# Optimization experiments

Measured on AMD Instinct MI355X. Metric: run time of the kernel, lower is better.

The kernel has to match this reference:

```python
import jax, jax.numpy as jnp
import numpy as np

NUM_HEADS = 8
HIDDEN_DIM = 64
N_REAL = 30000
N_VIRT = 2000
N_NODES = N_REAL + N_VIRT
N_EDGES = 512000
VOCAB = 100000


def setup_inputs() -> dict:
    key = jax.random.key(0)
    k1, k2, k3, k4, k5 = jax.random.split(key, 5)
    features = jax.random.normal(k1, (VOCAB, HIDDEN_DIM), dtype=jnp.float32)
    virtue_emb = jax.random.normal(k2, (N_VIRT, HIDDEN_DIM), dtype=jnp.float32)  # nn.Embedding weight ~ N(0,1)
    cnodes = jax.random.randint(k3, (N_REAL,), 0, VOCAB, dtype=jnp.int64)
    src = jax.random.randint(k4, (N_EDGES,), 0, N_NODES, dtype=jnp.int64)
    dst = jax.random.randint(k5, (N_EDGES,), 0, N_NODES, dtype=jnp.int64)
    vm_idx = jnp.arange(N_VIRT, dtype=jnp.int64) + N_REAL  # virtual nodes are appended after real nodes
    return {"features": features, "virtue_emb": virtue_emb, "cnodes": cnodes,
            "src": src, "dst": dst, "vm_idx": vm_idx}


def _edge_softmax(e, dst, n_nodes):
    # DGL edge_softmax: softmax over incoming edges of each destination node.
    m = jax.ops.segment_max(e, dst, num_segments=n_nodes)          # [N,H,1]
    ex = jnp.exp(e - m[dst])                                       # [E,H,1]
    s = jax.ops.segment_sum(ex, dst, num_segments=n_nodes)        # [N,H,1]
    return ex / s[dst]


def reference(features, virtue_emb, cnodes, src, dst, vm_idx):
    real_ndata = features[cnodes]                                  # [R,D] F.embedding
    ndata = jnp.concatenate([real_ndata, virtue_emb], axis=0)      # [N,D]
    n = ndata.shape[0]
    # agg_type='neighbor': cat([h]*H, dim=1).view(-1,H,D) == broadcast along head dim
    nft = jnp.broadcast_to(ndata[:, None, :], (n, NUM_HEADS, HIDDEN_DIM))
    e = jnp.ones((src.shape[0], NUM_HEADS, 1), dtype=ndata.dtype)
    eft = _edge_softmax(e, dst, n)                                 # [E,H,1]
    new_nft = jax.ops.segment_sum(nft[src] * eft, dst, num_segments=n)      # round 1: u_mul_e / sum
    final_nft = jax.ops.segment_sum(new_nft[src] * eft, dst, num_segments=n)  # round 2
    return final_nft[vm_idx]                                       # [V,H,D]
```

## Files before the change

### kernel.cpp

```cpp
#include <hip/hip_runtime.h>

constexpr int HEADS  = 8;
constexpr int DIM    = 64;
constexpr int NREAL  = 30000;
constexpr int NVIRT  = 2000;
constexpr int NNODES = NREAL + NVIRT;
constexpr int NEDGES = 512000;
constexpr int STRIDE = 64;


__global__ __launch_bounds__(256) void k_prep(const float* __restrict__ features,
                                              const float* __restrict__ virtue,
                                              const int* __restrict__ cnodes,
                                              const int* __restrict__ src,
                                              const int* __restrict__ dst,
                                              float* __restrict__ ndata,
                                              int* __restrict__ cnt,
                                              unsigned short* __restrict__ slots) {
  int i = blockIdx.x * blockDim.x + threadIdx.x;
  {
    int node = i >> 4;
    int q    = i & 15;
    const float4* srcp = (node < NREAL)
        ? (const float4*)(features + (long)cnodes[node] * DIM)
        : (const float4*)(virtue + (long)(node - NREAL) * DIM);
    ((float4*)(ndata + (long)node * DIM))[q] = srcp[q];
  }
  {
    int d = dst[i];
    int pos = atomicAdd(&cnt[d], 1);
    if (pos < STRIDE) slots[(long)d * STRIDE + pos] = (unsigned short)src[i];
  }
}

__global__ __launch_bounds__(256) void k_agg1(const int* __restrict__ cnt,
                                              const unsigned short* __restrict__ slots,
                                              const float* __restrict__ ndata,
                                              float* __restrict__ new_nft) {
  int node = blockIdx.x * 4 + (threadIdx.x >> 6);
  if (node >= NNODES) return;
  int lane = threadIdx.x & 63;
  int q = lane >> 4;
  int l = lane & 15;
  int deg = cnt[node];
  if (deg > STRIDE) deg = STRIDE;
  int myidx = 0;
  if (lane < deg) myidx = (int)slots[(long)node * STRIDE + lane];
  float4 acc  = make_float4(0.f, 0.f, 0.f, 0.f);
  float4 acc2 = make_float4(0.f, 0.f, 0.f, 0.f);
  const float4* nd4 = (const float4*)ndata;
  for (int k0 = 0; k0 < deg; k0 += 8) {
    int ka = k0 + q;
    int kb = k0 + q + 4;
    int sa = __shfl(myidx, ka);
    int sb = __shfl(myidx, kb);
    if (ka < deg) {
      float4 v = nd4[(long)sa * 16 + l];
      acc.x += v.x; acc.y += v.y; acc.z += v.z; acc.w += v.w;
    }
    if (kb < deg) {
      float4 v = nd4[(long)sb * 16 + l];
      acc2.x += v.x; acc2.y += v.y; acc2.z += v.z; acc2.w += v.w;
    }
  }
  acc.x += acc2.x; acc.y += acc2.y; acc.z += acc2.z; acc.w += acc2.w;
  acc.x += __shfl_xor(acc.x, 16); acc.y += __shfl_xor(acc.y, 16);
  acc.z += __shfl_xor(acc.z, 16); acc.w += __shfl_xor(acc.w, 16);
  acc.x += __shfl_xor(acc.x, 32); acc.y += __shfl_xor(acc.y, 32);
  acc.z += __shfl_xor(acc.z, 32); acc.w += __shfl_xor(acc.w, 32);
  if (q == 0) {
    float inv = (deg > 0) ? 1.0f / (float)deg : 0.0f;
    acc.x *= inv; acc.y *= inv; acc.z *= inv; acc.w *= inv;
    ((float4*)new_nft)[(long)node * 16 + l] = acc;
  }
}

__global__ __launch_bounds__(256) void k_agg2(const int* __restrict__ cnt,
                                              const unsigned short* __restrict__ slots,
                                              const float* __restrict__ new_nft,
                                              float* __restrict__ out) {
  int v = blockIdx.x * 4 + (threadIdx.x >> 6);
  if (v >= NVIRT) return;
  int node = NREAL + v;
  int lane = threadIdx.x & 63;
  int q = lane >> 4;
  int l = lane & 15;
  int deg = cnt[node];
  if (deg > STRIDE) deg = STRIDE;
  int myidx = 0;
  if (lane < deg) myidx = (int)slots[(long)node * STRIDE + lane];
  float4 acc  = make_float4(0.f, 0.f, 0.f, 0.f);
  float4 acc2 = make_float4(0.f, 0.f, 0.f, 0.f);
  const float4* nf4 = (const float4*)new_nft;
  for (int k0 = 0; k0 < deg; k0 += 8) {
    int ka = k0 + q;
    int kb = k0 + q + 4;
    int sa = __shfl(myidx, ka);
    int sb = __shfl(myidx, kb);
    if (ka < deg) {
      float4 x = nf4[(long)sa * 16 + l];
      acc.x += x.x; acc.y += x.y; acc.z += x.z; acc.w += x.w;
    }
    if (kb < deg) {
      float4 x = nf4[(long)sb * 16 + l];
      acc2.x += x.x; acc2.y += x.y; acc2.z += x.z; acc2.w += x.w;
    }
  }
  acc.x += acc2.x; acc.y += acc2.y; acc.z += acc2.z; acc.w += acc2.w;
  acc.x += __shfl_xor(acc.x, 16); acc.y += __shfl_xor(acc.y, 16);
  acc.z += __shfl_xor(acc.z, 16); acc.w += __shfl_xor(acc.w, 16);
  acc.x += __shfl_xor(acc.x, 32); acc.y += __shfl_xor(acc.y, 32);
  acc.z += __shfl_xor(acc.z, 32); acc.w += __shfl_xor(acc.w, 32);
  if (q == 0) {
    float inv = (deg > 0) ? 1.0f / (float)deg : 0.0f;
    acc.x *= inv; acc.y *= inv; acc.z *= inv; acc.w *= inv;
    float4* o4 = (float4*)out;
#pragma unroll
    for (int h = 0; h < HEADS; ++h)
      o4[((long)v * HEADS + h) * 16 + l] = acc;
  }
}


extern "C" void kernel_launch(void* const* d_in, const int* in_sizes, int n_in,
                              void* d_out, int out_size, void* d_ws, size_t ws_size,
                              hipStream_t stream) {
  const float* features = (const float*)d_in[0];
  const float* virtue   = (const float*)d_in[1];
  const int*   cnodes   = (const int*)d_in[2];
  const int*   src      = (const int*)d_in[3];
  const int*   dst      = (const int*)d_in[4];
  float* out = (float*)d_out;

  float*          ndata   = (float*)d_ws;
  float*          new_nft = ndata + (long)NNODES * DIM;
  int*            cnt     = (int*)(new_nft + (long)NNODES * DIM);
  unsigned short* slots   = (unsigned short*)(cnt + NNODES);

  const int B = 256;

  hipMemsetAsync(cnt, 0, NNODES * sizeof(int), stream);
  k_prep<<<NEDGES / B, B, 0, stream>>>(features, virtue, cnodes, src, dst,
                                       ndata, cnt, slots);
  k_agg1<<<(NNODES + 3) / 4, B, 0, stream>>>(cnt, slots, ndata, new_nft);
  k_agg2<<<(NVIRT + 3) / 4, B, 0, stream>>>(cnt, slots, new_nft, out);
}
```

Before: 134.4 us.

## Store node features in fp16 and skip round-1 nodes not feeding virtual nodes

Node features are stored as fp16 instead of fp32, which halves the bytes gathered in the first aggregation round. A byte mark array is also set in the prep kernel for every source node that has an edge into a virtual node, and the first aggregation skips all unmarked nodes because their results are never read. The costs are lost precision in the intermediate features and extra scattered byte writes during prep. About half of the nodes may still be marked given the average degree.

```diff
diff --git a/kernel.cpp b/kernel.cpp
--- a/kernel.cpp
+++ b/kernel.cpp
@@ -8,14 +8,17 @@
 constexpr int NEDGES = 512000;
 constexpr int STRIDE = 64;
 
+typedef _Float16 half4 __attribute__((ext_vector_type(4)));
+
 
 __global__ __launch_bounds__(256) void k_prep(const float* __restrict__ features,
                                               const float* __restrict__ virtue,
                                               const int* __restrict__ cnodes,
                                               const int* __restrict__ src,
                                               const int* __restrict__ dst,
-                                              float* __restrict__ ndata,
+                                              _Float16* __restrict__ ndata,
                                               int* __restrict__ cnt,
+                                              unsigned char* __restrict__ mark,
                                               unsigned short* __restrict__ slots) {
   int i = blockIdx.x * blockDim.x + threadIdx.x;
   {
@@ -24,21 +27,27 @@
     const float4* srcp = (node < NREAL)
         ? (const float4*)(features + (long)cnodes[node] * DIM)
         : (const float4*)(virtue + (long)(node - NREAL) * DIM);
-    ((float4*)(ndata + (long)node * DIM))[q] = srcp[q];
+    float4 v = srcp[q];
+    half4 h = { (_Float16)v.x, (_Float16)v.y, (_Float16)v.z, (_Float16)v.w };
+    ((half4*)(ndata + (long)node * DIM))[q] = h;
   }
   {
     int d = dst[i];
+    int s = src[i];
     int pos = atomicAdd(&cnt[d], 1);
-    if (pos < STRIDE) slots[(long)d * STRIDE + pos] = (unsigned short)src[i];
+    if (pos < STRIDE) slots[(long)d * STRIDE + pos] = (unsigned short)s;
+    if (d >= NREAL) mark[s] = 1;
   }
 }
 
 __global__ __launch_bounds__(256) void k_agg1(const int* __restrict__ cnt,
+                                              const unsigned char* __restrict__ mark,
                                               const unsigned short* __restrict__ slots,
-                                              const float* __restrict__ ndata,
+                                              const _Float16* __restrict__ ndata,
                                               float* __restrict__ new_nft) {
   int node = blockIdx.x * 4 + (threadIdx.x >> 6);
   if (node >= NNODES) return;
+  if (!mark[node]) return;
   int lane = threadIdx.x & 63;
   int q = lane >> 4;
   int l = lane & 15;
@@ -48,19 +57,19 @@
   if (lane < deg) myidx = (int)slots[(long)node * STRIDE + lane];
   float4 acc  = make_float4(0.f, 0.f, 0.f, 0.f);
   float4 acc2 = make_float4(0.f, 0.f, 0.f, 0.f);
-  const float4* nd4 = (const float4*)ndata;
+  const half4* nd = (const half4*)ndata;
   for (int k0 = 0; k0 < deg; k0 += 8) {
     int ka = k0 + q;
     int kb = k0 + q + 4;
     int sa = __shfl(myidx, ka);
     int sb = __shfl(myidx, kb);
     if (ka < deg) {
-      float4 v = nd4[(long)sa * 16 + l];
-      acc.x += v.x; acc.y += v.y; acc.z += v.z; acc.w += v.w;
+      half4 v = nd[(long)sa * 16 + l];
+      acc.x += (float)v.x; acc.y += (float)v.y; acc.z += (float)v.z; acc.w += (float)v.w;
     }
     if (kb < deg) {
-      float4 v = nd4[(long)sb * 16 + l];
-      acc2.x += v.x; acc2.y += v.y; acc2.z += v.z; acc2.w += v.w;
+      half4 v = nd[(long)sb * 16 + l];
+      acc2.x += (float)v.x; acc2.y += (float)v.y; acc2.z += (float)v.z; acc2.w += (float)v.w;
     }
   }
   acc.x += acc2.x; acc.y += acc2.y; acc.z += acc2.z; acc.w += acc2.w;
@@ -132,16 +141,17 @@
   const int*   dst      = (const int*)d_in[4];
   float* out = (float*)d_out;
 
-  float*          ndata   = (float*)d_ws;
-  float*          new_nft = ndata + (long)NNODES * DIM;
-  int*            cnt     = (int*)(new_nft + (long)NNODES * DIM);
-  unsigned short* slots   = (unsigned short*)(cnt + NNODES);
+  float*          new_nft = (float*)d_ws;
+  _Float16*       ndata   = (_Float16*)(new_nft + (long)NNODES * DIM);
+  int*            cnt     = (int*)(ndata + (long)NNODES * DIM);
+  unsigned char*  mark    = (unsigned char*)(cnt + NNODES);
+  unsigned short* slots   = (unsigned short*)(mark + NNODES);
 
   const int B = 256;
 
-  hipMemsetAsync(cnt, 0, NNODES * sizeof(int), stream);
+  hipMemsetAsync(cnt, 0, NNODES * sizeof(int) + NNODES, stream);
   k_prep<<<NEDGES / B, B, 0, stream>>>(features, virtue, cnodes, src, dst,
-                                       ndata, cnt, slots);
-  k_agg1<<<(NNODES + 3) / 4, B, 0, stream>>>(cnt, slots, ndata, new_nft);
+                                       ndata, cnt, mark, slots);
+  k_agg1<<<(NNODES + 3) / 4, B, 0, stream>>>(cnt, mark, slots, ndata, new_nft);
   k_agg2<<<(NVIRT + 3) / 4, B, 0, stream>>>(cnt, slots, new_nft, out);
 }
```

New measurement: 128.8 us. 4.1% less time.
